# Performance work log

Hardware: AMD Instinct MI355X
Metric: run time of the kernel (lower is better)

## Reference

```python
import jax, jax.numpy as jnp
import numpy as np

B, C, HK, WK = 1, 128, 32, 32
S = 4                       # upsample factor hq/hk = dilation
HQ, WQ = HK * S, WK * S
NH = 4                      # heads
HD = C // NH                # head dim
KH = KW = 7                 # odd(max(3, round(2*0.1*32)))
DH = DW = S
EPS = float(jnp.finfo(jnp.float32).eps)  # torch RMSNorm default eps for fp32


def natten_indices(L, K, D):
    """NATTEN clamped-window key indices per query position. Returns [L, K] int array."""
    NS = K // 2
    i = np.arange(L)
    if D <= 1:
        start = np.maximum(i - NS, 0) + (i + NS >= L) * (L - i - NS - 1)
    else:
        ni = i - NS * D
        imodd = i % D
        a = (L // D) * D
        b = L - a
        far = np.where(imodd < b, L - b + imodd - 2 * NS * D, a + imodd - K * D)
        start = np.where(ni < 0, imodd, np.where(i + NS * D >= L, far, ni))
    return jnp.asarray(start[:, None] + np.arange(K)[None, :] * D)


def setup_inputs() -> dict:
    key = jax.random.key(0)
    ks = jax.random.split(key, 8)
    sc = 1.0 / np.sqrt(C)
    return {
        "q": jax.random.normal(ks[0], (B, C, HQ, WQ), jnp.float32),
        "k": jax.random.normal(ks[1], (B, C, HK, WK), jnp.float32),
        "v": jax.random.normal(ks[2], (B, C, HK, WK), jnp.float32),
        "conv_w": jax.random.normal(ks[3], (C, C, 3, 3), jnp.float32) * (sc / 3.0),
        "normq_w": 1.0 + 0.02 * jax.random.normal(ks[4], (C,), jnp.float32),
        "normk_w": 1.0 + 0.02 * jax.random.normal(ks[5], (C,), jnp.float32),
        "qproj_w": jax.random.normal(ks[6], (C, C), jnp.float32) * sc,
        "qproj_b": jnp.zeros((C,), jnp.float32),
        "kproj_w": jax.random.normal(ks[7], (C, C), jnp.float32) * sc,
        "kproj_b": jnp.zeros((C,), jnp.float32),
    }


def _rmsnorm(x, w):  # x: [B,C,H,W]; RMS over channel dim
    ms = jnp.mean(x * x, axis=1, keepdims=True)
    return x * jax.lax.rsqrt(ms + EPS) * w[None, :, None, None]


def reference(q, k, v, conv_w, normq_w, normk_w, qproj_w, qproj_b, kproj_w, kproj_b):
    # 3x3 conv on q (no bias, padding=1)
    q = jax.lax.conv_general_dilated(q, conv_w, (1, 1), "SAME",
                                     dimension_numbers=("NCHW", "OIHW", "NCHW"))
    q = _rmsnorm(q, normq_w)
    k = _rmsnorm(k, normk_w)
    # 1x1 projections (Conv2d k=1 with bias)
    q = jnp.einsum("oc,bchw->bohw", qproj_w, q) + qproj_b[None, :, None, None]
    k = jnp.einsum("oc,bchw->bohw", kproj_w, k) + kproj_b[None, :, None, None]
    # nearest-exact upsample of k, v to (HQ, WQ); integer factor -> exact pixel repeat
    k = jnp.repeat(jnp.repeat(k, S, axis=2), S, axis=3)
    v = jnp.repeat(jnp.repeat(v, S, axis=2), S, axis=3)
    # NATTEN layout [B, H, W, heads, hd]
    qn = q.reshape(B, NH, HD, HQ, WQ).transpose(0, 3, 4, 1, 2)
    kn = k.reshape(B, NH, HD, HQ, WQ).transpose(0, 3, 4, 1, 2)
    vh = v.transpose(0, 2, 3, 1)  # [B,HQ,WQ,C]; V is shared (expanded) across heads.
    # channel-pad-to-8 in the original is a no-op here since C % 8 == 0.
    ih = natten_indices(HQ, KH, DH)  # [HQ, KH]
    iw = natten_indices(WQ, KW, DW)  # [WQ, KW]
    k_nb = jnp.take(jnp.take(kn, ih, axis=1), iw, axis=3)  # [B,HQ,KH,WQ,KW,NH,HD]
    v_nb = jnp.take(jnp.take(vh, ih, axis=1), iw, axis=3)  # [B,HQ,KH,WQ,KW,C]
    scale = HD ** -0.5
    logits = jnp.einsum("bijhd,bimjnhd->bijhmn", qn, k_nb) * scale
    attn = jax.nn.softmax(logits.reshape(B, HQ, WQ, NH, KH * KW), axis=-1)
    attn = attn.reshape(B, HQ, WQ, NH, KH, KW)
    # heads share V, and the block takes mean over heads at the end; the mean
    # commutes with the (linear) V-contraction, so average attention first.
    attn_mean = attn.mean(axis=3)  # [B,HQ,WQ,KH,KW]
    out = jnp.einsum("bijmn,bimjnc->bcij", attn_mean, v_nb)  # [B,C,HQ,WQ]
    return out
```

## Files before the change

### kernel.cpp

```cpp
#include <hip/hip_runtime.h>

#define EPS_ 1.1920928955078125e-07f
#define SCALE_ 0.17677669529663687f

typedef __attribute__((ext_vector_type(8))) short s8b;
typedef __attribute__((ext_vector_type(4))) float f32x4;

static __device__ __forceinline__ unsigned short f2bf(float f) {
  unsigned int u = __float_as_uint(f);
  unsigned int r = (u + 0x7fffu + ((u >> 16) & 1u)) >> 16;
  return (unsigned short)r;
}
static __device__ __forceinline__ float b2fs(short h) {
  return __uint_as_float(((unsigned int)(unsigned short)h) << 16);
}
static __device__ __forceinline__ int S_(int c) {
  return (c < 3) ? 0 : ((c > 28) ? 25 : (c - 3));
}

__global__ __launch_bounds__(512) void prep_k(
    const float* __restrict__ k_in, const float* __restrict__ v_in,
    const float* __restrict__ conv_w, const float* __restrict__ normq_w,
    const float* __restrict__ normk_w, const float* __restrict__ qproj_w,
    const float* __restrict__ kproj_w, const float* __restrict__ kbias,
    unsigned short* __restrict__ vb, unsigned short* __restrict__ kpb,
    unsigned short* __restrict__ wb, unsigned short* __restrict__ wnq) {
  __shared__ __align__(16) char smem[54528];
  const int b = blockIdx.x, tid = threadIdx.x;
  const int w = tid >> 6, lane = tid & 63;
  const int lm = lane & 15, kg = lane >> 4;
  const int wm = w >> 1, wn = w & 1;

  if (b < 16) {
    unsigned short* x_l = (unsigned short*)smem;
    unsigned short* wnk_l = (unsigned short*)(smem + 17408);
    float* red_l = (float*)(smem + 52224);
    float* rs_l  = (float*)(smem + 54272);
    const int px0 = b * 64;
    for (int i = tid; i < 2048; i += 512) {
      int c = i >> 4, f = i & 15;
      float4 v = *(const float4*)&k_in[c * 1024 + px0 + f * 4];
      x_l[(f * 4 + 0) * 136 + c] = f2bf(v.x);
      x_l[(f * 4 + 1) * 136 + c] = f2bf(v.y);
      x_l[(f * 4 + 2) * 136 + c] = f2bf(v.z);
      x_l[(f * 4 + 3) * 136 + c] = f2bf(v.w);
    }
    for (int i = tid; i < 16384; i += 512) {
      int o = i >> 7, c = i & 127;
      wnk_l[o * 136 + c] = f2bf(kproj_w[i] * normk_w[c]);
    }
    __syncthreads();
    {
      int px = tid >> 3, t8 = tid & 7;
      float ssum = 0.f;
#pragma unroll
      for (int j = 0; j < 2; j++) {
        s8b v = *(const s8b*)&x_l[px * 136 + t8 * 16 + j * 8];
#pragma unroll
        for (int e = 0; e < 8; e++) { float f = b2fs(v[e]); ssum += f * f; }
      }
      red_l[px * 8 + t8] = ssum;
    }
    __syncthreads();
    if (tid < 64) {
      float4 r0 = *(const float4*)&red_l[tid * 8];
      float4 r1 = *(const float4*)&red_l[tid * 8 + 4];
      rs_l[tid] = rsqrtf((r0.x + r0.y + r0.z + r0.w + r1.x + r1.y + r1.z + r1.w) *
                             (1.f / 128.f) + EPS_);
    }
    __syncthreads();
    f32x4 acc[2][2];
#pragma unroll
    for (int a = 0; a < 2; a++)
#pragma unroll
      for (int n = 0; n < 2; n++) acc[a][n] = (f32x4){0.f, 0.f, 0.f, 0.f};
#pragma unroll
    for (int kc = 0; kc < 4; kc++) {
      s8b a0 = *(const s8b*)&wnk_l[(wm * 32 + lm) * 136 + kc * 32 + kg * 8];
      s8b a1 = *(const s8b*)&wnk_l[(wm * 32 + 16 + lm) * 136 + kc * 32 + kg * 8];
#pragma unroll
      for (int ni = 0; ni < 2; ni++) {
        s8b bf = *(const s8b*)&x_l[((wn * 2 + ni) * 16 + lm) * 136 + kc * 32 + kg * 8];
        acc[0][ni] = __builtin_amdgcn_mfma_f32_16x16x32_bf16(a0, bf, acc[0][ni], 0, 0, 0);
        acc[1][ni] = __builtin_amdgcn_mfma_f32_16x16x32_bf16(a1, bf, acc[1][ni], 0, 0, 0);
      }
    }
    __syncthreads();
#pragma unroll
    for (int mi = 0; mi < 2; mi++)
#pragma unroll
      for (int ni = 0; ni < 2; ni++)
#pragma unroll
        for (int r = 0; r < 4; r++) {
          int px = (wn * 2 + ni) * 16 + lm, c = wm * 32 + mi * 16 + kg * 4 + r;
          x_l[px * 136 + c] = f2bf(kbias[c] + rs_l[px] * acc[mi][ni][r]);
        }
    __syncthreads();
    for (int i = tid; i < 1024; i += 512) {
      int px = i >> 4, s = i & 15;
      *(s8b*)&kpb[(px0 + px) * 128 + s * 8] = *(const s8b*)&x_l[px * 136 + s * 8];
    }
  } else if (b < 48) {
    int g = (b - 16) * 512 + tid;
    int i32 = g & 31, oc = (g >> 5) & 127, kc = g >> 12;
    const float* src = conv_w + oc * 1152 + (kc * 32 + i32) * 9;
#pragma unroll
    for (int t = 0; t < 9; t++)
      wb[t * 16384 + g] = f2bf(src[t]);
  } else if (b < 56) {
#pragma unroll
    for (int it = 0; it < 4; it++) {
      int ch8 = (b - 48) * 2048 + it * 512 + tid;
      const float4 v0 = *(const float4*)&v_in[ch8 * 8];
      const float4 v1 = *(const float4*)&v_in[ch8 * 8 + 4];
      s8b o;
      o[0] = (short)f2bf(v0.x); o[1] = (short)f2bf(v0.y);
      o[2] = (short)f2bf(v0.z); o[3] = (short)f2bf(v0.w);
      o[4] = (short)f2bf(v1.x); o[5] = (short)f2bf(v1.y);
      o[6] = (short)f2bf(v1.z); o[7] = (short)f2bf(v1.w);
      *(s8b*)&vb[ch8 * 8] = o;
    }
  } else {
    int base = ((b - 56) * 512 + tid) * 8;
    const float4 v0 = *(const float4*)&qproj_w[base];
    const float4 v1 = *(const float4*)&qproj_w[base + 4];
    int c = base & 127;
    s8b o;
    o[0] = (short)f2bf(v0.x * normq_w[c + 0]); o[1] = (short)f2bf(v0.y * normq_w[c + 1]);
    o[2] = (short)f2bf(v0.z * normq_w[c + 2]); o[3] = (short)f2bf(v0.w * normq_w[c + 3]);
    o[4] = (short)f2bf(v1.x * normq_w[c + 4]); o[5] = (short)f2bf(v1.y * normq_w[c + 5]);
    o[6] = (short)f2bf(v1.z * normq_w[c + 6]); o[7] = (short)f2bf(v1.w * normq_w[c + 7]);
    *(s8b*)&wnq[base] = o;
  }
}

__global__ __launch_bounds__(512, 2) void fused_k(
    const float* __restrict__ q_in, const unsigned short* __restrict__ wb,
    const unsigned short* __restrict__ wnq, const float* __restrict__ qbias,
    const unsigned short* __restrict__ kpb, const unsigned short* __restrict__ vb,
    float* __restrict__ out) {
  __shared__ __align__(16) char smem[54272];
  unsigned short* in_l = (unsigned short*)smem;
  unsigned short* qc_l = (unsigned short*)smem;
  unsigned short* a_l  = (unsigned short*)smem;
  float* o_l = (float*)smem;
  unsigned short* v_l = (unsigned short*)(smem + 34816);
  float* red_l = (float*)(smem + 53248);

  const int tid = threadIdx.x;
  const int CY = blockIdx.x >> 4, CX = blockIdx.x & 15;
  const int Y0 = CY * 8, X0 = CX * 8;
  const int w = tid >> 6, lane = tid & 63;
  const int lm = lane & 15, kg = lane >> 4;
  const int wm = w >> 1, wn = w & 1;

  const int sy0 = S_(2 * CY), sy1 = S_(2 * CY + 1);
  const int sx0 = S_(2 * CX), sx1 = S_(2 * CX + 1);
  const int kyb = min(sy0, 24), kxb = min(sx0, 24);
  const int oy0 = sy0 - kyb, oy1 = sy1 - kyb;
  const int ox0 = sx0 - kxb, ox1 = sx1 - kxb;

  const int h = w >> 1, qh = w & 1;
  s8b bfv[4];
#pragma unroll
  for (int nt = 0; nt < 4; nt++) {
    int n = nt * 16 + lm;
    int ky = n >> 3, kx = n & 7;
    bfv[nt] = *(const s8b*)&kpb[((kyb + ky) * 32 + kxb + kx) * 128 + h * 32 + kg * 8];
  }
  s8b wq0[4], wq1[4];
#pragma unroll
  for (int kc = 0; kc < 4; kc++) {
    wq0[kc] = *(const s8b*)&wnq[(wm * 32 + lm) * 128 + kc * 32 + kg * 8];
    wq1[kc] = *(const s8b*)&wnq[(wm * 32 + 16 + lm) * 128 + kc * 32 + kg * 8];
  }
  float4 qbv[2];
  qbv[0] = *(const float4*)&qbias[wm * 32 + kg * 4];
  qbv[1] = *(const float4*)&qbias[wm * 32 + 16 + kg * 4];

  for (int i = tid; i < 5120; i += 512) {
    int j = i & 3, r = i >> 2;
    int ch = r & 127, ry = r >> 7;
    int y = Y0 - 1 + ry;
    int col0 = X0 - 4 + 4 * j;
    float4 v = {0.f, 0.f, 0.f, 0.f};
    if ((unsigned)y < 128u && (unsigned)col0 < 125u)
      v = *(const float4*)&q_in[ch * 16384 + y * 128 + col0];
    int rxb = 4 * j - 3;
#pragma unroll
    for (int e = 0; e < 4; e++) {
      int rx = rxb + e;
      if ((unsigned)rx < 10u)
        in_l[(ry * 12 + rx) * 136 + ch] = f2bf(((const float*)&v)[e]);
    }
  }
  {
    const int kxe = kxb & ~1;
    for (int i = tid; i < 1024; i += 512) {
      int ch = i & 127, ky = i >> 7;
      const unsigned short* src = &vb[ch * 1024 + (kyb + ky) * 32 + kxe];
      s8b a = *(const s8b*)src;
      if (kxb & 1) {
        s8b bsec = *(const s8b*)(src + 8);
        s8b o;
#pragma unroll
        for (int e = 0; e < 7; e++) o[e] = a[e + 1];
        o[7] = bsec[0];
        *(s8b*)&v_l[ch * 72 + ky * 8] = o;
      } else {
        *(s8b*)&v_l[ch * 72 + ky * 8] = a;
      }
    }
  }
  __syncthreads();

  f32x4 acc[2][2];
#pragma unroll
  for (int a = 0; a < 2; a++)
#pragma unroll
    for (int n = 0; n < 2; n++) acc[a][n] = (f32x4){0.f, 0.f, 0.f, 0.f};
  {
    s8b wa0 = *(const s8b*)&wb[(wm * 32 + lm) * 32 + kg * 8];
    s8b wa1 = *(const s8b*)&wb[(wm * 32 + 16 + lm) * 32 + kg * 8];
#pragma unroll
    for (int idx = 0; idx < 36; idx++) {
      s8b na0 = wa0, na1 = wa1;
      if (idx < 35) {
        const unsigned short* wp = wb + (idx + 1) * 4096;
        na0 = *(const s8b*)&wp[(wm * 32 + lm) * 32 + kg * 8];
        na1 = *(const s8b*)&wp[(wm * 32 + 16 + lm) * 32 + kg * 8];
      }
      const int t = idx >> 2, kc = idx & 3;
      const int dy = t / 3, dx = t - (t / 3) * 3;
#pragma unroll
      for (int ni = 0; ni < 2; ni++) {
        int nt = wn * 2 + ni;
        int qy = 2 * nt + (lm >> 3), qx = lm & 7;
        s8b bf = *(const s8b*)&in_l[((qy + dy) * 12 + qx + dx) * 136 + kc * 32 + kg * 8];
        acc[0][ni] = __builtin_amdgcn_mfma_f32_16x16x32_bf16(wa0, bf, acc[0][ni], 0, 0, 0);
        acc[1][ni] = __builtin_amdgcn_mfma_f32_16x16x32_bf16(wa1, bf, acc[1][ni], 0, 0, 0);
      }
      wa0 = na0; wa1 = na1;
    }
  }
  {
    float ss[2] = {0.f, 0.f};
#pragma unroll
    for (int mi = 0; mi < 2; mi++)
#pragma unroll
      for (int ni = 0; ni < 2; ni++)
#pragma unroll
        for (int r = 0; r < 4; r++) {
          float v = acc[mi][ni][r];
          ss[ni] += v * v;
          int px = (wn * 2 + ni) * 16 + lm, c = wm * 32 + mi * 16 + kg * 4 + r;
          qc_l[px * 136 + c] = f2bf(v);
        }
#pragma unroll
    for (int ni = 0; ni < 2; ni++) {
      ss[ni] += __shfl_xor(ss[ni], 16, 64);
      ss[ni] += __shfl_xor(ss[ni], 32, 64);
    }
    if (kg == 0) {
      red_l[((wn * 2 + 0) * 16 + lm) * 4 + wm] = ss[0];
      red_l[((wn * 2 + 1) * 16 + lm) * 4 + wm] = ss[1];
    }
  }
  __syncthreads();

  f32x4 acc2[2][2];
#pragma unroll
  for (int a = 0; a < 2; a++)
#pragma unroll
    for (int n = 0; n < 2; n++) acc2[a][n] = (f32x4){0.f, 0.f, 0.f, 0.f};
#pragma unroll
  for (int kc = 0; kc < 4; kc++) {
#pragma unroll
    for (int ni = 0; ni < 2; ni++) {
      s8b bf = *(const s8b*)&qc_l[((wn * 2 + ni) * 16 + lm) * 136 + kc * 32 + kg * 8];
      acc2[0][ni] = __builtin_amdgcn_mfma_f32_16x16x32_bf16(wq0[kc], bf, acc2[0][ni], 0, 0, 0);
      acc2[1][ni] = __builtin_amdgcn_mfma_f32_16x16x32_bf16(wq1[kc], bf, acc2[1][ni], 0, 0, 0);
    }
  }
  __syncthreads();
#pragma unroll
  for (int ni = 0; ni < 2; ni++) {
    int px = (wn * 2 + ni) * 16 + lm;
    float4 rr = *(const float4*)&red_l[px * 4];
    float rs = rsqrtf((rr.x + rr.y + rr.z + rr.w) * (1.f / 128.f) + EPS_);
#pragma unroll
    for (int mi = 0; mi < 2; mi++)
#pragma unroll
      for (int r = 0; r < 4; r++) {
        int c = wm * 32 + mi * 16 + kg * 4 + r;
        qc_l[px * 136 + c] = f2bf(((const float*)&qbv[mi])[r] + rs * acc2[mi][ni][r]);
      }
  }

  f32x4 lg[2][4];
  {
    s8b af[2];
#pragma unroll
    for (int i = 0; i < 2; i++)
      af[i] = *(const s8b*)&qc_l[((qh * 2 + i) * 16 + lm) * 136 + h * 32 + kg * 8];
#pragma unroll
    for (int i = 0; i < 2; i++)
#pragma unroll
      for (int nt = 0; nt < 4; nt++)
        lg[i][nt] = __builtin_amdgcn_mfma_f32_16x16x32_bf16(
            af[i], bfv[nt], (f32x4){0.f, 0.f, 0.f, 0.f}, 0, 0, 0);
  }
  __syncthreads();

  const int kyA = lm >> 3, kxq = lm & 7;
  const bool kxv0 = (unsigned)(kxq - ox0) < 7u;
  const bool kxv1 = (unsigned)(kxq - ox1) < 7u;
#pragma unroll
  for (int i = 0; i < 2; i++) {
    const int mt = qh * 2 + i;
#pragma unroll
    for (int r = 0; r < 4; r++) {
      int j = mt * 16 + kg * 4 + r;
      int oy = ((j >> 5) & 1) ? oy1 : oy0;
      bool kxv = ((j >> 2) & 1) ? kxv1 : kxv0;
      float l[4];
#pragma unroll
      for (int nt = 0; nt < 4; nt++) {
        int ky = 2 * nt + kyA;
        bool valid = kxv && ((unsigned)(ky - oy) < 7u);
        l[nt] = valid ? lg[i][nt][r] * SCALE_ : -1e30f;
      }
      float mx = fmaxf(fmaxf(l[0], l[1]), fmaxf(l[2], l[3]));
#pragma unroll
      for (int off = 1; off < 16; off <<= 1) mx = fmaxf(mx, __shfl_xor(mx, off, 64));
      float e0 = __expf(l[0] - mx), e1 = __expf(l[1] - mx);
      float e2 = __expf(l[2] - mx), e3 = __expf(l[3] - mx);
      float ss = e0 + e1 + e2 + e3;
#pragma unroll
      for (int off = 1; off < 16; off <<= 1) ss += __shfl_xor(ss, off, 64);
      float inv = 1.f / ss;
      unsigned short* ap = &a_l[(h * 64 + j) * 68];
      ap[lm] = f2bf(e0 * inv);
      ap[16 + lm] = f2bf(e1 * inv);
      ap[32 + lm] = f2bf(e2 * inv);
      ap[48 + lm] = f2bf(e3 * inv);
    }
  }
  __syncthreads();

  const int ph = w & 1, cb = w >> 1;
  f32x4 oacc[2][2];
#pragma unroll
  for (int a = 0; a < 2; a++)
#pragma unroll
    for (int n = 0; n < 2; n++) oacc[a][n] = (f32x4){0.f, 0.f, 0.f, 0.f};
#pragma unroll
  for (int kc = 0; kc < 2; kc++) {
    s8b bfr[2];
#pragma unroll
    for (int nt2 = 0; nt2 < 2; nt2++)
      bfr[nt2] = *(const s8b*)&v_l[(cb * 32 + nt2 * 16 + lm) * 72 + kc * 32 + kg * 8];
#pragma unroll
    for (int hh = 0; hh < 4; hh++) {
#pragma unroll
      for (int mi = 0; mi < 2; mi++) {
        s8b afr = *(const s8b*)&a_l[(hh * 64 + (ph * 2 + mi) * 16 + lm) * 68 + kc * 32 + kg * 8];
#pragma unroll
        for (int nt2 = 0; nt2 < 2; nt2++)
          oacc[mi][nt2] = __builtin_amdgcn_mfma_f32_16x16x32_bf16(afr, bfr[nt2], oacc[mi][nt2], 0, 0, 0);
      }
    }
  }
  __syncthreads();
#pragma unroll
  for (int mi = 0; mi < 2; mi++)
#pragma unroll
    for (int nt2 = 0; nt2 < 2; nt2++)
#pragma unroll
      for (int r = 0; r < 4; r++)
        o_l[(cb * 32 + nt2 * 16 + lm) * 68 + (ph * 2 + mi) * 16 + kg * 4 + r] =
            0.25f * oacc[mi][nt2][r];
  __syncthreads();
  for (int i = tid; i < 2048; i += 512) {
    int c = i >> 4, rr = i & 15;
    int qy = rr >> 1, hx = rr & 1;
    float4 v = *(const float4*)&o_l[c * 68 + qy * 8 + hx * 4];
    *(float4*)&out[c * 16384 + (Y0 + qy) * 128 + X0 + hx * 4] = v;
  }
}

extern "C" void kernel_launch(void* const* d_in, const int* in_sizes, int n_in,
                              void* d_out, int out_size, void* d_ws, size_t ws_size,
                              hipStream_t stream) {
  const float* q_in    = (const float*)d_in[0];
  const float* k_in    = (const float*)d_in[1];
  const float* v_in    = (const float*)d_in[2];
  const float* conv_w  = (const float*)d_in[3];
  const float* normq_w = (const float*)d_in[4];
  const float* normk_w = (const float*)d_in[5];
  const float* qproj_w = (const float*)d_in[6];
  const float* qproj_b = (const float*)d_in[7];
  const float* kproj_w = (const float*)d_in[8];
  const float* kproj_b = (const float*)d_in[9];
  float* out = (float*)d_out;

  char* ws = (char*)d_ws;
  unsigned short* vb  = (unsigned short*)(ws);
  unsigned short* kpb = (unsigned short*)(ws + 262144);
  unsigned short* wb  = (unsigned short*)(ws + 524288);
  unsigned short* wnq = (unsigned short*)(ws + 819200);

  prep_k<<<dim3(60), 512, 0, stream>>>(k_in, v_in, conv_w, normq_w, normk_w,
                                       qproj_w, kproj_w, kproj_b,
                                       vb, kpb, wb, wnq);
  fused_k<<<dim3(256), 512, 0, stream>>>(q_in, wb, wnq, qproj_b, kpb, vb, out);
}
```

Baseline: 112.1 us.

## Split fused conv+attention kernel into separate conv and attention kernels

Splits the single fused kernel into a conv/RMSNorm/projection kernel that writes projected q in bf16 to workspace, and an attention kernel over 4x8 tiles with 256 threads and 512 blocks. The goal is more blocks and better occupancy for the attention phase, and dropping its kernel-wide syncs. The cost is an extra kernel launch and a global round trip of the q tensor (128x128x128 bf16).

```diff
diff --git a/kernel.cpp b/kernel.cpp
--- a/kernel.cpp
+++ b/kernel.cpp
@@ -134,18 +134,14 @@
   }
 }
 
-__global__ __launch_bounds__(512, 2) void fused_k(
+__global__ __launch_bounds__(512, 2) void conv_k(
     const float* __restrict__ q_in, const unsigned short* __restrict__ wb,
     const unsigned short* __restrict__ wnq, const float* __restrict__ qbias,
-    const unsigned short* __restrict__ kpb, const unsigned short* __restrict__ vb,
-    float* __restrict__ out) {
-  __shared__ __align__(16) char smem[54272];
+    unsigned short* __restrict__ qpb) {
+  __shared__ __align__(16) char smem[51072];
   unsigned short* in_l = (unsigned short*)smem;
-  unsigned short* qc_l = (unsigned short*)smem;
-  unsigned short* a_l  = (unsigned short*)smem;
-  float* o_l = (float*)smem;
-  unsigned short* v_l = (unsigned short*)(smem + 34816);
-  float* red_l = (float*)(smem + 53248);
+  unsigned short* qc_l = (unsigned short*)(smem + 32640);
+  float* red_l = (float*)(smem + 50048);
 
   const int tid = threadIdx.x;
   const int CY = blockIdx.x >> 4, CX = blockIdx.x & 15;
@@ -154,20 +150,6 @@
   const int lm = lane & 15, kg = lane >> 4;
   const int wm = w >> 1, wn = w & 1;
 
-  const int sy0 = S_(2 * CY), sy1 = S_(2 * CY + 1);
-  const int sx0 = S_(2 * CX), sx1 = S_(2 * CX + 1);
-  const int kyb = min(sy0, 24), kxb = min(sx0, 24);
-  const int oy0 = sy0 - kyb, oy1 = sy1 - kyb;
-  const int ox0 = sx0 - kxb, ox1 = sx1 - kxb;
-
-  const int h = w >> 1, qh = w & 1;
-  s8b bfv[4];
-#pragma unroll
-  for (int nt = 0; nt < 4; nt++) {
-    int n = nt * 16 + lm;
-    int ky = n >> 3, kx = n & 7;
-    bfv[nt] = *(const s8b*)&kpb[((kyb + ky) * 32 + kxb + kx) * 128 + h * 32 + kg * 8];
-  }
   s8b wq0[4], wq1[4];
 #pragma unroll
   for (int kc = 0; kc < 4; kc++) {
@@ -194,9 +176,132 @@
         in_l[(ry * 12 + rx) * 136 + ch] = f2bf(((const float*)&v)[e]);
     }
   }
+  __syncthreads();
+
+  f32x4 acc[2][2];
+#pragma unroll
+  for (int a = 0; a < 2; a++)
+#pragma unroll
+    for (int n = 0; n < 2; n++) acc[a][n] = (f32x4){0.f, 0.f, 0.f, 0.f};
+  {
+    s8b wa0 = *(const s8b*)&wb[(wm * 32 + lm) * 32 + kg * 8];
+    s8b wa1 = *(const s8b*)&wb[(wm * 32 + 16 + lm) * 32 + kg * 8];
+#pragma unroll
+    for (int idx = 0; idx < 36; idx++) {
+      s8b na0 = wa0, na1 = wa1;
+      if (idx < 35) {
+        const unsigned short* wp = wb + (idx + 1) * 4096;
+        na0 = *(const s8b*)&wp[(wm * 32 + lm) * 32 + kg * 8];
+        na1 = *(const s8b*)&wp[(wm * 32 + 16 + lm) * 32 + kg * 8];
+      }
+      const int t = idx >> 2, kc = idx & 3;
+      const int dy = t / 3, dx = t - (t / 3) * 3;
+#pragma unroll
+      for (int ni = 0; ni < 2; ni++) {
+        int nt = wn * 2 + ni;
+        int qy = 2 * nt + (lm >> 3), qx = lm & 7;
+        s8b bf = *(const s8b*)&in_l[((qy + dy) * 12 + qx + dx) * 136 + kc * 32 + kg * 8];
+        acc[0][ni] = __builtin_amdgcn_mfma_f32_16x16x32_bf16(wa0, bf, acc[0][ni], 0, 0, 0);
+        acc[1][ni] = __builtin_amdgcn_mfma_f32_16x16x32_bf16(wa1, bf, acc[1][ni], 0, 0, 0);
+      }
+      wa0 = na0; wa1 = na1;
+    }
+  }
+  {
+    float ss[2] = {0.f, 0.f};
+#pragma unroll
+    for (int mi = 0; mi < 2; mi++)
+#pragma unroll
+      for (int ni = 0; ni < 2; ni++)
+#pragma unroll
+        for (int r = 0; r < 4; r++) {
+          float v = acc[mi][ni][r];
+          ss[ni] += v * v;
+          int px = (wn * 2 + ni) * 16 + lm, c = wm * 32 + mi * 16 + kg * 4 + r;
+          qc_l[px * 136 + c] = f2bf(v);
+        }
+#pragma unroll
+    for (int ni = 0; ni < 2; ni++) {
+      ss[ni] += __shfl_xor(ss[ni], 16, 64);
+      ss[ni] += __shfl_xor(ss[ni], 32, 64);
+    }
+    if (kg == 0) {
+      red_l[((wn * 2 + 0) * 16 + lm) * 4 + wm] = ss[0];
+      red_l[((wn * 2 + 1) * 16 + lm) * 4 + wm] = ss[1];
+    }
+  }
+  __syncthreads();
+
+  f32x4 acc2[2][2];
+#pragma unroll
+  for (int a = 0; a < 2; a++)
+#pragma unroll
+    for (int n = 0; n < 2; n++) acc2[a][n] = (f32x4){0.f, 0.f, 0.f, 0.f};
+#pragma unroll
+  for (int kc = 0; kc < 4; kc++) {
+#pragma unroll
+    for (int ni = 0; ni < 2; ni++) {
+      s8b bf = *(const s8b*)&qc_l[((wn * 2 + ni) * 16 + lm) * 136 + kc * 32 + kg * 8];
+      acc2[0][ni] = __builtin_amdgcn_mfma_f32_16x16x32_bf16(wq0[kc], bf, acc2[0][ni], 0, 0, 0);
+      acc2[1][ni] = __builtin_amdgcn_mfma_f32_16x16x32_bf16(wq1[kc], bf, acc2[1][ni], 0, 0, 0);
+    }
+  }
+#pragma unroll
+  for (int ni = 0; ni < 2; ni++) {
+    int px = (wn * 2 + ni) * 16 + lm;
+    float4 rr = *(const float4*)&red_l[px * 4];
+    float rs = rsqrtf((rr.x + rr.y + rr.z + rr.w) * (1.f / 128.f) + EPS_);
+    int gpx = (Y0 + (px >> 3)) * 128 + X0 + (px & 7);
+#pragma unroll
+    for (int mi = 0; mi < 2; mi++) {
+      unsigned int lo = (unsigned int)f2bf(((const float*)&qbv[mi])[0] + rs * acc2[mi][ni][0]) |
+                        ((unsigned int)f2bf(((const float*)&qbv[mi])[1] + rs * acc2[mi][ni][1]) << 16);
+      unsigned int hi = (unsigned int)f2bf(((const float*)&qbv[mi])[2] + rs * acc2[mi][ni][2]) |
+                        ((unsigned int)f2bf(((const float*)&qbv[mi])[3] + rs * acc2[mi][ni][3]) << 16);
+      uint2 pk = {lo, hi};
+      *(uint2*)&qpb[gpx * 128 + wm * 32 + mi * 16 + kg * 4] = pk;
+    }
+  }
+}
+
+__global__ __launch_bounds__(256, 2) void attn_k(
+    const unsigned short* __restrict__ qpb, const unsigned short* __restrict__ kpb,
+    const unsigned short* __restrict__ vb, float* __restrict__ out) {
+  __shared__ __align__(16) char smem[44544];
+  unsigned short* q_l = (unsigned short*)smem;
+  unsigned short* a_l = (unsigned short*)(smem + 8704);
+  unsigned short* v_l = (unsigned short*)(smem + 26112);
+  float* o_l = (float*)smem;
+
+  const int tid = threadIdx.x;
+  const int CY2 = blockIdx.x >> 4, CX = blockIdx.x & 15;
+  const int Y0 = CY2 * 4, X0 = CX * 8;
+  const int w = tid >> 6, lane = tid & 63;
+  const int lm = lane & 15, kg = lane >> 4;
+
+  const int sy = S_(CY2);
+  const int sx0 = S_(2 * CX), sx1 = S_(2 * CX + 1);
+  const int kyb = min(sy, 24), kxb = min(sx0, 24);
+  const int oy = sy - kyb;
+  const int ox0 = sx0 - kxb, ox1 = sx1 - kxb;
+
+  const int h = w;
+  s8b bfv[4];
+#pragma unroll
+  for (int nt = 0; nt < 4; nt++) {
+    int n = nt * 16 + lm;
+    int ky = n >> 3, kx = n & 7;
+    bfv[nt] = *(const s8b*)&kpb[((kyb + ky) * 32 + kxb + kx) * 128 + h * 32 + kg * 8];
+  }
+
+  for (int i = tid; i < 512; i += 256) {
+    int p = i >> 4, s = i & 15;
+    int gpx = (Y0 + (p >> 3)) * 128 + X0 + (p & 7);
+    *(s8b*)&q_l[p * 136 + s * 8] = *(const s8b*)&qpb[gpx * 128 + s * 8];
+  }
   {
     const int kxe = kxb & ~1;
-    for (int i = tid; i < 1024; i += 512) {
+    for (int i = tid; i < 1024; i += 256) {
       int ch = i & 127, ky = i >> 7;
       const unsigned short* src = &vb[ch * 1024 + (kyb + ky) * 32 + kxe];
       s8b a = *(const s8b*)src;
@@ -214,95 +319,12 @@
   }
   __syncthreads();
 
-  f32x4 acc[2][2];
-#pragma unroll
-  for (int a = 0; a < 2; a++)
-#pragma unroll
-    for (int n = 0; n < 2; n++) acc[a][n] = (f32x4){0.f, 0.f, 0.f, 0.f};
-  {
-    s8b wa0 = *(const s8b*)&wb[(wm * 32 + lm) * 32 + kg * 8];
-    s8b wa1 = *(const s8b*)&wb[(wm * 32 + 16 + lm) * 32 + kg * 8];
-#pragma unroll
-    for (int idx = 0; idx < 36; idx++) {
-      s8b na0 = wa0, na1 = wa1;
-      if (idx < 35) {
-        const unsigned short* wp = wb + (idx + 1) * 4096;
-        na0 = *(const s8b*)&wp[(wm * 32 + lm) * 32 + kg * 8];
-        na1 = *(const s8b*)&wp[(wm * 32 + 16 + lm) * 32 + kg * 8];
-      }
-      const int t = idx >> 2, kc = idx & 3;
-      const int dy = t / 3, dx = t - (t / 3) * 3;
-#pragma unroll
-      for (int ni = 0; ni < 2; ni++) {
-        int nt = wn * 2 + ni;
-        int qy = 2 * nt + (lm >> 3), qx = lm & 7;
-        s8b bf = *(const s8b*)&in_l[((qy + dy) * 12 + qx + dx) * 136 + kc * 32 + kg * 8];
-        acc[0][ni] = __builtin_amdgcn_mfma_f32_16x16x32_bf16(wa0, bf, acc[0][ni], 0, 0, 0);
-        acc[1][ni] = __builtin_amdgcn_mfma_f32_16x16x32_bf16(wa1, bf, acc[1][ni], 0, 0, 0);
-      }
-      wa0 = na0; wa1 = na1;
-    }
-  }
-  {
-    float ss[2] = {0.f, 0.f};
-#pragma unroll
-    for (int mi = 0; mi < 2; mi++)
-#pragma unroll
-      for (int ni = 0; ni < 2; ni++)
-#pragma unroll
-        for (int r = 0; r < 4; r++) {
-          float v = acc[mi][ni][r];
-          ss[ni] += v * v;
-          int px = (wn * 2 + ni) * 16 + lm, c = wm * 32 + mi * 16 + kg * 4 + r;
-          qc_l[px * 136 + c] = f2bf(v);
-        }
-#pragma unroll
-    for (int ni = 0; ni < 2; ni++) {
-      ss[ni] += __shfl_xor(ss[ni], 16, 64);
-      ss[ni] += __shfl_xor(ss[ni], 32, 64);
-    }
-    if (kg == 0) {
-      red_l[((wn * 2 + 0) * 16 + lm) * 4 + wm] = ss[0];
-      red_l[((wn * 2 + 1) * 16 + lm) * 4 + wm] = ss[1];
-    }
-  }
-  __syncthreads();
-
-  f32x4 acc2[2][2];
-#pragma unroll
-  for (int a = 0; a < 2; a++)
-#pragma unroll
-    for (int n = 0; n < 2; n++) acc2[a][n] = (f32x4){0.f, 0.f, 0.f, 0.f};
-#pragma unroll
-  for (int kc = 0; kc < 4; kc++) {
-#pragma unroll
-    for (int ni = 0; ni < 2; ni++) {
-      s8b bf = *(const s8b*)&qc_l[((wn * 2 + ni) * 16 + lm) * 136 + kc * 32 + kg * 8];
-      acc2[0][ni] = __builtin_amdgcn_mfma_f32_16x16x32_bf16(wq0[kc], bf, acc2[0][ni], 0, 0, 0);
-      acc2[1][ni] = __builtin_amdgcn_mfma_f32_16x16x32_bf16(wq1[kc], bf, acc2[1][ni], 0, 0, 0);
-    }
-  }
-  __syncthreads();
-#pragma unroll
-  for (int ni = 0; ni < 2; ni++) {
-    int px = (wn * 2 + ni) * 16 + lm;
-    float4 rr = *(const float4*)&red_l[px * 4];
-    float rs = rsqrtf((rr.x + rr.y + rr.z + rr.w) * (1.f / 128.f) + EPS_);
-#pragma unroll
-    for (int mi = 0; mi < 2; mi++)
-#pragma unroll
-      for (int r = 0; r < 4; r++) {
-        int c = wm * 32 + mi * 16 + kg * 4 + r;
-        qc_l[px * 136 + c] = f2bf(((const float*)&qbv[mi])[r] + rs * acc2[mi][ni][r]);
-      }
-  }
-
   f32x4 lg[2][4];
   {
     s8b af[2];
 #pragma unroll
     for (int i = 0; i < 2; i++)
-      af[i] = *(const s8b*)&qc_l[((qh * 2 + i) * 16 + lm) * 136 + h * 32 + kg * 8];
+      af[i] = *(const s8b*)&q_l[(i * 16 + lm) * 136 + h * 32 + kg * 8];
 #pragma unroll
     for (int i = 0; i < 2; i++)
 #pragma unroll
@@ -310,19 +332,16 @@
         lg[i][nt] = __builtin_amdgcn_mfma_f32_16x16x32_bf16(
             af[i], bfv[nt], (f32x4){0.f, 0.f, 0.f, 0.f}, 0, 0, 0);
   }
-  __syncthreads();
 
   const int kyA = lm >> 3, kxq = lm & 7;
   const bool kxv0 = (unsigned)(kxq - ox0) < 7u;
   const bool kxv1 = (unsigned)(kxq - ox1) < 7u;
 #pragma unroll
   for (int i = 0; i < 2; i++) {
-    const int mt = qh * 2 + i;
 #pragma unroll
     for (int r = 0; r < 4; r++) {
-      int j = mt * 16 + kg * 4 + r;
-      int oy = ((j >> 5) & 1) ? oy1 : oy0;
-      bool kxv = ((j >> 2) & 1) ? kxv1 : kxv0;
+      int q = i * 16 + kg * 4 + r;
+      bool kxv = (kg & 1) ? kxv1 : kxv0;
       float l[4];
 #pragma unroll
       for (int nt = 0; nt < 4; nt++) {
@@ -339,7 +358,7 @@
 #pragma unroll
       for (int off = 1; off < 16; off <<= 1) ss += __shfl_xor(ss, off, 64);
       float inv = 1.f / ss;
-      unsigned short* ap = &a_l[(h * 64 + j) * 68];
+      unsigned short* ap = &a_l[(h * 32 + q) * 68];
       ap[lm] = f2bf(e0 * inv);
       ap[16 + lm] = f2bf(e1 * inv);
       ap[32 + lm] = f2bf(e2 * inv);
@@ -348,7 +367,6 @@
   }
   __syncthreads();
 
-  const int ph = w & 1, cb = w >> 1;
   f32x4 oacc[2][2];
 #pragma unroll
   for (int a = 0; a < 2; a++)
@@ -359,32 +377,31 @@
     s8b bfr[2];
 #pragma unroll
     for (int nt2 = 0; nt2 < 2; nt2++)
-      bfr[nt2] = *(const s8b*)&v_l[(cb * 32 + nt2 * 16 + lm) * 72 + kc * 32 + kg * 8];
+      bfr[nt2] = *(const s8b*)&v_l[(w * 32 + nt2 * 16 + lm) * 72 + kc * 32 + kg * 8];
 #pragma unroll
     for (int hh = 0; hh < 4; hh++) {
 #pragma unroll
-      for (int mi = 0; mi < 2; mi++) {
-        s8b afr = *(const s8b*)&a_l[(hh * 64 + (ph * 2 + mi) * 16 + lm) * 68 + kc * 32 + kg * 8];
+      for (int mt = 0; mt < 2; mt++) {
+        s8b afr = *(const s8b*)&a_l[(hh * 32 + mt * 16 + lm) * 68 + kc * 32 + kg * 8];
 #pragma unroll
         for (int nt2 = 0; nt2 < 2; nt2++)
-          oacc[mi][nt2] = __builtin_amdgcn_mfma_f32_16x16x32_bf16(afr, bfr[nt2], oacc[mi][nt2], 0, 0, 0);
-      }
-    }
-  }
-  __syncthreads();
-#pragma unroll
-  for (int mi = 0; mi < 2; mi++)
+          oacc[mt][nt2] = __builtin_amdgcn_mfma_f32_16x16x32_bf16(afr, bfr[nt2], oacc[mt][nt2], 0, 0, 0);
+      }
+    }
+  }
+  __syncthreads();
+#pragma unroll
+  for (int mt = 0; mt < 2; mt++)
 #pragma unroll
     for (int nt2 = 0; nt2 < 2; nt2++)
 #pragma unroll
       for (int r = 0; r < 4; r++)
-        o_l[(cb * 32 + nt2 * 16 + lm) * 68 + (ph * 2 + mi) * 16 + kg * 4 + r] =
-            0.25f * oacc[mi][nt2][r];
-  __syncthreads();
-  for (int i = tid; i < 2048; i += 512) {
-    int c = i >> 4, rr = i & 15;
+        o_l[(w * 32 + nt2 * 16 + lm) * 36 + mt * 16 + kg * 4 + r] = 0.25f * oacc[mt][nt2][r];
+  __syncthreads();
+  for (int i = tid; i < 1024; i += 256) {
+    int c = i >> 3, rr = i & 7;
     int qy = rr >> 1, hx = rr & 1;
-    float4 v = *(const float4*)&o_l[c * 68 + qy * 8 + hx * 4];
+    float4 v = *(const float4*)&o_l[c * 36 + qy * 8 + hx * 4];
     *(float4*)&out[c * 16384 + (Y0 + qy) * 128 + X0 + hx * 4] = v;
   }
 }
@@ -409,9 +426,11 @@
   unsigned short* kpb = (unsigned short*)(ws + 262144);
   unsigned short* wb  = (unsigned short*)(ws + 524288);
   unsigned short* wnq = (unsigned short*)(ws + 819200);
+  unsigned short* qpb = (unsigned short*)(ws + 851968);
 
   prep_k<<<dim3(60), 512, 0, stream>>>(k_in, v_in, conv_w, normq_w, normk_w,
                                        qproj_w, kproj_w, kproj_b,
                                        vb, kpb, wb, wnq);
-  fused_k<<<dim3(256), 512, 0, stream>>>(q_in, wb, wnq, qproj_b, kpb, vb, out);
-}
+  conv_k<<<dim3(256), 512, 0, stream>>>(q_in, wb, wnq, qproj_b, qpb);
+  attn_k<<<dim3(512), 256, 0, stream>>>(qpb, kpb, vb, out);
+}
```

Result: slower. 114.5 us (+2.2%).

## Pre-transpose q to padded channel-last bf16 buffer in prep kernel

Applied to the files above, without the earlier changes.

Adds 128 blocks to the prep kernel that convert q from fp32 NCHW into a bf16 channel-last buffer with a one-pixel zero border (130x130), plus blocks that zero the border. The fused kernel then loads its conv halo tile with 16-byte vector copies and no bounds checks, instead of strided fp32 loads with per-element conversion and transposed shared-memory scatter. This trades an extra full pass over q (a global write and re-read of about 4 MB) for cheaper, coalesced tile loads in the main kernel. A barrier is also added after the conv loop.

```diff
diff --git a/kernel.cpp b/kernel.cpp
--- a/kernel.cpp
+++ b/kernel.cpp
@@ -19,24 +19,48 @@
 }
 
 __global__ __launch_bounds__(512) void prep_k(
-    const float* __restrict__ k_in, const float* __restrict__ v_in,
-    const float* __restrict__ conv_w, const float* __restrict__ normq_w,
-    const float* __restrict__ normk_w, const float* __restrict__ qproj_w,
-    const float* __restrict__ kproj_w, const float* __restrict__ kbias,
-    unsigned short* __restrict__ vb, unsigned short* __restrict__ kpb,
-    unsigned short* __restrict__ wb, unsigned short* __restrict__ wnq) {
+    const float* __restrict__ q_in, const float* __restrict__ k_in,
+    const float* __restrict__ v_in, const float* __restrict__ conv_w,
+    const float* __restrict__ normq_w, const float* __restrict__ normk_w,
+    const float* __restrict__ qproj_w, const float* __restrict__ kproj_w,
+    const float* __restrict__ kbias,
+    unsigned short* __restrict__ qb, unsigned short* __restrict__ vb,
+    unsigned short* __restrict__ kpb, unsigned short* __restrict__ wb,
+    unsigned short* __restrict__ wnq) {
   __shared__ __align__(16) char smem[54528];
   const int b = blockIdx.x, tid = threadIdx.x;
   const int w = tid >> 6, lane = tid & 63;
   const int lm = lane & 15, kg = lane >> 4;
   const int wm = w >> 1, wn = w & 1;
 
-  if (b < 16) {
+  if (b < 128) {
+    unsigned short* t_l = (unsigned short*)smem;
+#pragma unroll
+    for (int u = 0; u < 2; u++) {
+      const int px0 = b * 128 + u * 64;
+      for (int i = tid; i < 2048; i += 512) {
+        int c = i >> 4, f = i & 15;
+        float4 v = *(const float4*)&q_in[c * 16384 + px0 + f * 4];
+        t_l[(f * 4 + 0) * 136 + c] = f2bf(v.x);
+        t_l[(f * 4 + 1) * 136 + c] = f2bf(v.y);
+        t_l[(f * 4 + 2) * 136 + c] = f2bf(v.z);
+        t_l[(f * 4 + 3) * 136 + c] = f2bf(v.w);
+      }
+      __syncthreads();
+      for (int i = tid; i < 1024; i += 512) {
+        int p = i >> 4, s = i & 15;
+        int px = px0 + p;
+        int opx = px + 2 * (px >> 7) + 131;
+        *(s8b*)&qb[opx * 128 + s * 8] = *(const s8b*)&t_l[p * 136 + s * 8];
+      }
+      __syncthreads();
+    }
+  } else if (b < 144) {
     unsigned short* x_l = (unsigned short*)smem;
     unsigned short* wnk_l = (unsigned short*)(smem + 17408);
     float* red_l = (float*)(smem + 52224);
     float* rs_l  = (float*)(smem + 54272);
-    const int px0 = b * 64;
+    const int px0 = (b - 128) * 64;
     for (int i = tid; i < 2048; i += 512) {
       int c = i >> 4, f = i & 15;
       float4 v = *(const float4*)&k_in[c * 1024 + px0 + f * 4];
@@ -100,17 +124,17 @@
       int px = i >> 4, s = i & 15;
       *(s8b*)&kpb[(px0 + px) * 128 + s * 8] = *(const s8b*)&x_l[px * 136 + s * 8];
     }
-  } else if (b < 48) {
-    int g = (b - 16) * 512 + tid;
+  } else if (b < 176) {
+    int g = (b - 144) * 512 + tid;
     int i32 = g & 31, oc = (g >> 5) & 127, kc = g >> 12;
     const float* src = conv_w + oc * 1152 + (kc * 32 + i32) * 9;
 #pragma unroll
     for (int t = 0; t < 9; t++)
       wb[t * 16384 + g] = f2bf(src[t]);
-  } else if (b < 56) {
+  } else if (b < 184) {
 #pragma unroll
     for (int it = 0; it < 4; it++) {
-      int ch8 = (b - 48) * 2048 + it * 512 + tid;
+      int ch8 = (b - 176) * 2048 + it * 512 + tid;
       const float4 v0 = *(const float4*)&v_in[ch8 * 8];
       const float4 v1 = *(const float4*)&v_in[ch8 * 8 + 4];
       s8b o;
@@ -120,8 +144,8 @@
       o[6] = (short)f2bf(v1.z); o[7] = (short)f2bf(v1.w);
       *(s8b*)&vb[ch8 * 8] = o;
     }
-  } else {
-    int base = ((b - 56) * 512 + tid) * 8;
+  } else if (b < 188) {
+    int base = ((b - 184) * 512 + tid) * 8;
     const float4 v0 = *(const float4*)&qproj_w[base];
     const float4 v1 = *(const float4*)&qproj_w[base + 4];
     int c = base & 127;
@@ -131,11 +155,23 @@
     o[4] = (short)f2bf(v1.x * normq_w[c + 4]); o[5] = (short)f2bf(v1.y * normq_w[c + 5]);
     o[6] = (short)f2bf(v1.z * normq_w[c + 6]); o[7] = (short)f2bf(v1.w * normq_w[c + 7]);
     *(s8b*)&wnq[base] = o;
+  } else {
+    int gid = (b - 188) * 512 + tid;
+    s8b z = {0, 0, 0, 0, 0, 0, 0, 0};
+    if (gid < 2080) {
+      *(s8b*)&qb[gid * 8] = z;
+      *(s8b*)&qb[129 * 130 * 128 + gid * 8] = z;
+    }
+    if (gid < 2048) {
+      int r = (gid >> 4) + 1, s = gid & 15;
+      *(s8b*)&qb[(r * 130) * 128 + s * 8] = z;
+      *(s8b*)&qb[(r * 130 + 129) * 128 + s * 8] = z;
+    }
   }
 }
 
 __global__ __launch_bounds__(512, 2) void fused_k(
-    const float* __restrict__ q_in, const unsigned short* __restrict__ wb,
+    const unsigned short* __restrict__ qb, const unsigned short* __restrict__ wb,
     const unsigned short* __restrict__ wnq, const float* __restrict__ qbias,
     const unsigned short* __restrict__ kpb, const unsigned short* __restrict__ vb,
     float* __restrict__ out) {
@@ -178,21 +214,11 @@
   qbv[0] = *(const float4*)&qbias[wm * 32 + kg * 4];
   qbv[1] = *(const float4*)&qbias[wm * 32 + 16 + kg * 4];
 
-  for (int i = tid; i < 5120; i += 512) {
-    int j = i & 3, r = i >> 2;
-    int ch = r & 127, ry = r >> 7;
-    int y = Y0 - 1 + ry;
-    int col0 = X0 - 4 + 4 * j;
-    float4 v = {0.f, 0.f, 0.f, 0.f};
-    if ((unsigned)y < 128u && (unsigned)col0 < 125u)
-      v = *(const float4*)&q_in[ch * 16384 + y * 128 + col0];
-    int rxb = 4 * j - 3;
-#pragma unroll
-    for (int e = 0; e < 4; e++) {
-      int rx = rxb + e;
-      if ((unsigned)rx < 10u)
-        in_l[(ry * 12 + rx) * 136 + ch] = f2bf(((const float*)&v)[e]);
-    }
+  for (int i = tid; i < 1600; i += 512) {
+    int s = i & 15, r = i >> 4;
+    int ry = r / 10, rx = r - ry * 10;
+    *(s8b*)&in_l[(ry * 12 + rx) * 136 + s * 8] =
+        *(const s8b*)&qb[((Y0 + ry) * 130 + X0 + rx) * 128 + s * 8];
   }
   {
     const int kxe = kxb & ~1;
@@ -243,6 +269,8 @@
       wa0 = na0; wa1 = na1;
     }
   }
+  __syncthreads();
+
   {
     float ss[2] = {0.f, 0.f};
 #pragma unroll
@@ -405,13 +433,14 @@
   float* out = (float*)d_out;
 
   char* ws = (char*)d_ws;
-  unsigned short* vb  = (unsigned short*)(ws);
-  unsigned short* kpb = (unsigned short*)(ws + 262144);
-  unsigned short* wb  = (unsigned short*)(ws + 524288);
-  unsigned short* wnq = (unsigned short*)(ws + 819200);
-
-  prep_k<<<dim3(60), 512, 0, stream>>>(k_in, v_in, conv_w, normq_w, normk_w,
-                                       qproj_w, kproj_w, kproj_b,
-                                       vb, kpb, wb, wnq);
-  fused_k<<<dim3(256), 512, 0, stream>>>(q_in, wb, wnq, qproj_b, kpb, vb, out);
-}
+  unsigned short* qb  = (unsigned short*)(ws);
+  unsigned short* vb  = (unsigned short*)(ws + 4326400);
+  unsigned short* kpb = (unsigned short*)(ws + 4588544);
+  unsigned short* wb  = (unsigned short*)(ws + 4850688);
+  unsigned short* wnq = (unsigned short*)(ws + 5145600);
+
+  prep_k<<<dim3(193), 512, 0, stream>>>(q_in, k_in, v_in, conv_w, normq_w, normk_w,
+                                        qproj_w, kproj_w, kproj_b,
+                                        qb, vb, kpb, wb, wnq);
+  fused_k<<<dim3(256), 512, 0, stream>>>(qb, wb, wnq, qproj_b, kpb, vb, out);
+}
```

Result: faster. 105.3 us (-6.0%).
